# Kernel tuning notes

Hardware: AMD Instinct MI355X
Metric: run time of the kernel (lower is better)

The kernel has to match this reference:

```python
import jax, jax.numpy as jnp
import numpy as np

IN_FEATURE = 512
HID = 1024
N_EXPERTS = 16


def setup_inputs() -> dict:
    key = jax.random.key(0)
    ks = jax.random.split(key, 13)
    s_in = 1.0 / np.sqrt(IN_FEATURE)
    s_hid = 1.0 / np.sqrt(HID)
    x = jax.random.normal(ks[0], (8192, IN_FEATURE), dtype=jnp.float32)
    # Stacked expert params: expert i is Linear(in,hid)->silu->Linear(hid,hid)->silu->Linear(hid,1)
    W1 = jax.random.uniform(ks[1], (N_EXPERTS, IN_FEATURE, HID), jnp.float32, -s_in, s_in)
    b1 = jax.random.uniform(ks[2], (N_EXPERTS, HID), jnp.float32, -s_in, s_in)
    W2 = jax.random.uniform(ks[3], (N_EXPERTS, HID, HID), jnp.float32, -s_hid, s_hid)
    b2 = jax.random.uniform(ks[4], (N_EXPERTS, HID), jnp.float32, -s_hid, s_hid)
    W3 = jax.random.uniform(ks[5], (N_EXPERTS, HID), jnp.float32, -s_hid, s_hid)  # Linear(hid,1) weight, squeezed
    b3 = jax.random.uniform(ks[6], (N_EXPERTS,), jnp.float32, -s_hid, s_hid)
    # Gating params
    Wg1 = jax.random.uniform(ks[7], (IN_FEATURE, HID), jnp.float32, -s_in, s_in)
    bg1 = jax.random.uniform(ks[8], (HID,), jnp.float32, -s_in, s_in)
    Wg2 = jax.random.uniform(ks[9], (HID, HID), jnp.float32, -s_hid, s_hid)
    bg2 = jax.random.uniform(ks[10], (HID,), jnp.float32, -s_hid, s_hid)
    Wg3 = jax.random.uniform(ks[11], (HID, N_EXPERTS), jnp.float32, -s_hid, s_hid)
    bg3 = jax.random.uniform(ks[12], (N_EXPERTS,), jnp.float32, -s_hid, s_hid)
    return {"x": x, "W1": W1, "b1": b1, "W2": W2, "b2": b2, "W3": W3, "b3": b3,
            "Wg1": Wg1, "bg1": bg1, "Wg2": Wg2, "bg2": bg2, "Wg3": Wg3, "bg3": bg3}


def reference(x, W1, b1, W2, b2, W3, b3, Wg1, bg1, Wg2, bg2, Wg3, bg3):
    act = jax.nn.silu
    # Experts, batched over the expert axis: h [B, E, H]
    h = act(jnp.einsum('bi,eih->beh', x, W1) + b1)
    h = act(jnp.einsum('beh,ehk->bek', h, W2) + b2)
    expert_out = jnp.einsum('bek,ek->be', h, W3) + b3  # [B, E]
    # Gating network -> softmax over experts
    g = act(x @ Wg1 + bg1)
    g = act(g @ Wg2 + bg2)
    gate = jax.nn.softmax(g @ Wg3 + bg3, axis=1)  # [B, E]
    final = jnp.sum(expert_out * gate, axis=1).reshape(-1, 1)  # [B, 1]
    return final
```

## Files before the change

### kernel.cpp

```cpp
#include <hip/hip_runtime.h>

#define TOKENS 8192
#define INF 512
#define HIDDEN 1024
#define NEXP 16

typedef short bh4 __attribute__((ext_vector_type(4)));
typedef short bh8 __attribute__((ext_vector_type(8)));
typedef float f32x4 __attribute__((ext_vector_type(4)));

__device__ __forceinline__ short f2b(float f) {
  union { float f; unsigned u; } v; v.f = f;
  unsigned r = v.u + 0x7FFFu + ((v.u >> 16) & 1u);
  return (short)(r >> 16);
}
__device__ __forceinline__ float b2f(short h) {
  union { unsigned u; float f; } v; v.u = ((unsigned)(unsigned short)h) << 16;
  return v.f;
}
__device__ __forceinline__ float silu_f(float x) { return x / (1.f + __expf(-x)); }

__device__ __forceinline__ f32x4 mfma_16x16x32_bf16(bh8 a, bh8 b, f32x4 c) {
  asm("v_mfma_f32_16x16x32_bf16 %0, %1, %2, %0" : "+v"(c) : "v"(a), "v"(b));
  return c;
}

__global__ __launch_bounds__(256) void prep_kernel(
    const float* __restrict__ x, short* __restrict__ xb,
    const float* __restrict__ W1, short* __restrict__ W1t,
    const float* __restrict__ W2, short* __restrict__ W2t,
    const float* __restrict__ Wg1, short* __restrict__ Wg1t,
    const float* __restrict__ Wg2, short* __restrict__ Wg2t,
    float* __restrict__ eout) {
  __shared__ float tile[32][33];
  const int b = blockIdx.x;
  const int tid = threadIdx.x;

  if (b < 1024) {
    int nv = (TOKENS * INF) >> 2;
    int stride = 1024 * 256;
    for (int i = b * 256 + tid; i < nv; i += stride) {
      float4 v = ((const float4*)x)[i];
      bh4 o;
      o[0] = f2b(v.x); o[1] = f2b(v.y); o[2] = f2b(v.z); o[3] = f2b(v.w);
      *(bh4*)(xb + (size_t)i * 4) = o;
    }
    return;
  }
  if (b >= 27136) {
    int i = (b - 27136) * 256 + tid;
    f32x4 z; z[0] = 0.f; z[1] = 0.f; z[2] = 0.f; z[3] = 0.f;
    *(f32x4*)&eout[(size_t)i * 4] = z;
    return;
  }

  const float* src; short* dst; int R, C, bx, by; bool piDst;
  if (b < 9216) {
    int s = b - 1024; int zz = s >> 9; int rem = s & 511;
    bx = rem & 31; by = rem >> 5; R = INF; C = HIDDEN; piDst = false;
    src = W1 + (size_t)zz * R * C; dst = W1t + (size_t)zz * R * C;
  } else if (b < 25600) {
    int s = b - 9216; int zz = s >> 10; int rem = s & 1023;
    bx = rem & 31; by = rem >> 5; R = HIDDEN; C = HIDDEN; piDst = true;
    src = W2 + (size_t)zz * R * C; dst = W2t + (size_t)zz * R * C;
  } else if (b < 26112) {
    int s = b - 25600; bx = s & 31; by = s >> 5; R = INF; C = HIDDEN; piDst = false;
    src = Wg1; dst = Wg1t;
  } else {
    int s = b - 26112; bx = s & 31; by = s >> 5; R = HIDDEN; C = HIDDEN; piDst = true;
    src = Wg2; dst = Wg2t;
  }
  const int c0 = bx * 32, r0 = by * 32;
  {
    const int row = tid >> 3, col4 = (tid & 7) * 4;
    float4 v = *(const float4*)&src[(size_t)(r0 + row) * C + (c0 + col4)];
    tile[row][col4 + 0] = v.x; tile[row][col4 + 1] = v.y;
    tile[row][col4 + 2] = v.z; tile[row][col4 + 3] = v.w;
  }
  __syncthreads();
  {
    const int dc = tid >> 3, g = tid & 7;
    bh4 o;
    o[0] = f2b(tile[4 * g + 0][dc]); o[1] = f2b(tile[4 * g + 1][dc]);
    o[2] = f2b(tile[4 * g + 2][dc]); o[3] = f2b(tile[4 * g + 3][dc]);
    const int base = piDst ? ((g & 3) * 8 + (g >> 2) * 4) : (4 * g);
    *(bh4*)&dst[(size_t)(c0 + dc) * R + r0 + base] = o;
  }
}

__global__ __launch_bounds__(256, 4) void gemm_moe(
    const short* __restrict__ Abase, size_t aStride,
    const short* __restrict__ BtE, const short* __restrict__ BtG, size_t bStride,
    const float* __restrict__ biasE, const float* __restrict__ biasG,
    short* __restrict__ Cbase, size_t cStride,
    const float* __restrict__ W3all, float* __restrict__ eout,
    int jobBase, int K, int phase) {
  __shared__ short As[128][64];
  __shared__ short Bs[128][64];
  const int z = blockIdx.z;
  const int job = jobBase + z;
  const short* A = Abase + (size_t)z * aStride;
  const short* Bt = (job < NEXP) ? BtE + (size_t)job * bStride : BtG;
  const float* bias = (job < NEXP) ? biasE + (size_t)job * HIDDEN : biasG;

  const int bx = blockIdx.x, by = blockIdx.y;
  const int n0 = (by >> 3) * 128;
  const int m0 = (bx * 8 + (by & 7)) * 128;

  const int tid = threadIdx.x;
  const int lane = tid & 63;
  const int wid = tid >> 6;
  const int wm = (wid >> 1) * 64;
  const int wn = (wid & 1) * 64;
  const int quad = lane >> 4;
  const int l15 = lane & 15;

  f32x4 acc[4][4];
  #pragma unroll
  for (int i = 0; i < 4; ++i)
    #pragma unroll
    for (int j = 0; j < 4; ++j) {
      acc[i][j][0] = 0.f; acc[i][j][1] = 0.f; acc[i][j][2] = 0.f; acc[i][j][3] = 0.f;
    }

  const int srow = lane >> 3;
  const int scol = ((lane & 7) << 3) ^ (srow << 3);
  const short* aBase = A + (size_t)(m0 + wid * 32 + srow) * K + scol;
  const short* bBase = Bt + (size_t)(n0 + wid * 32 + srow) * K + scol;
  char* ldsA = (char*)&As[0][0];
  char* ldsB = (char*)&Bs[0][0];

  for (int kt = 0; kt < K; kt += 64) {
    __syncthreads();
    #pragma unroll
    for (int i = 0; i < 4; ++i) {
      __builtin_amdgcn_global_load_lds(
          (const __attribute__((address_space(1))) void*)(aBase + (size_t)(i * 8) * K + kt),
          (__attribute__((address_space(3))) void*)(ldsA + (wid * 4 + i) * 1024), 16, 0, 0);
      __builtin_amdgcn_global_load_lds(
          (const __attribute__((address_space(1))) void*)(bBase + (size_t)(i * 8) * K + kt),
          (__attribute__((address_space(3))) void*)(ldsB + (wid * 4 + i) * 1024), 16, 0, 0);
    }
    __syncthreads();

    #pragma unroll
    for (int ks = 0; ks < 2; ++ks) {
      bh8 af[4], bfr[4];
      #pragma unroll
      for (int mi = 0; mi < 4; ++mi) {
        int row = wm + mi * 16 + l15;
        int col = ((ks << 5) + (quad << 3)) ^ ((row & 7) << 3);
        af[mi] = *(const bh8*)&As[row][col];
      }
      #pragma unroll
      for (int ni = 0; ni < 4; ++ni) {
        int row = wn + ni * 16 + l15;
        int col = ((ks << 5) + (quad << 3)) ^ ((row & 7) << 3);
        bfr[ni] = *(const bh8*)&Bs[row][col];
      }
      #pragma unroll
      for (int mi = 0; mi < 4; ++mi)
        #pragma unroll
        for (int ni = 0; ni < 4; ++ni)
          acc[mi][ni] = mfma_16x16x32_bf16(bfr[ni], af[mi], acc[mi][ni]);
    }
  }

  if (phase == 1) {
    short* C = Cbase + (size_t)z * cStride;
    f32x4 bv4[4];
    #pragma unroll
    for (int ni = 0; ni < 4; ++ni)
      bv4[ni] = *(const f32x4*)&bias[n0 + wn + ni * 16 + quad * 4];
    #pragma unroll
    for (int mi = 0; mi < 4; ++mi) {
      int mrow = m0 + wm + mi * 16 + l15;
      #pragma unroll
      for (int blk = 0; blk < 2; ++blk) {
        bh8 o;
        #pragma unroll
        for (int r = 0; r < 4; ++r) {
          o[r]     = f2b(silu_f(acc[mi][blk * 2 + 0][r] + bv4[blk * 2 + 0][r]));
          o[r + 4] = f2b(silu_f(acc[mi][blk * 2 + 1][r] + bv4[blk * 2 + 1][r]));
        }
        *(bh8*)&C[(size_t)mrow * HIDDEN + n0 + wn + blk * 32 + quad * 8] = o;
      }
    }
  } else if (job == NEXP) {
    short* C = Cbase;
    #pragma unroll
    for (int ni = 0; ni < 4; ++ni) {
      int nb = wn + ni * 16 + quad * 4;
      float4 bv4 = *(const float4*)&bias[n0 + nb];
      #pragma unroll
      for (int mi = 0; mi < 4; ++mi) {
        int mrow = m0 + wm + mi * 16 + l15;
        bh4 o;
        o[0] = f2b(silu_f(acc[mi][ni][0] + bv4.x));
        o[1] = f2b(silu_f(acc[mi][ni][1] + bv4.y));
        o[2] = f2b(silu_f(acc[mi][ni][2] + bv4.z));
        o[3] = f2b(silu_f(acc[mi][ni][3] + bv4.w));
        *(bh4*)&C[(size_t)mrow * HIDDEN + n0 + nb] = o;
      }
    }
  } else {
    const float* w3 = W3all + (size_t)job * HIDDEN;
    float4 bv4[4], wv4[4];
    #pragma unroll
    for (int ni = 0; ni < 4; ++ni) {
      int nb = n0 + wn + ni * 16 + quad * 4;
      bv4[ni] = *(const float4*)&bias[nb];
      wv4[ni] = *(const float4*)&w3[nb];
    }
    #pragma unroll
    for (int mi = 0; mi < 4; ++mi) {
      float s = 0.f;
      #pragma unroll
      for (int ni = 0; ni < 4; ++ni) {
        s += silu_f(acc[mi][ni][0] + bv4[ni].x) * wv4[ni].x;
        s += silu_f(acc[mi][ni][1] + bv4[ni].y) * wv4[ni].y;
        s += silu_f(acc[mi][ni][2] + bv4[ni].z) * wv4[ni].z;
        s += silu_f(acc[mi][ni][3] + bv4[ni].w) * wv4[ni].w;
      }
      s += __shfl_xor(s, 16);
      s += __shfl_xor(s, 32);
      if (quad == 0) {
        int mrow = m0 + wm + mi * 16 + l15;
        atomicAdd(&eout[(size_t)mrow * NEXP + job], s);
      }
    }
  }
}

__global__ __launch_bounds__(256) void final_kernel(
    const short* __restrict__ g2b, const float* __restrict__ Wg3,
    const float* __restrict__ bg3, const float* __restrict__ eout,
    const float* __restrict__ b3, float* __restrict__ out) {
  int wave = (blockIdx.x * 256 + threadIdx.x) >> 6;
  int lane = threadIdx.x & 63;
  int r0 = wave * 4;
  float lp[4][16];
  #pragma unroll
  for (int r = 0; r < 4; ++r)
    #pragma unroll
    for (int j = 0; j < 16; ++j) lp[r][j] = 0.f;

  for (int t = 0; t < HIDDEN / 64; ++t) {
    int k = t * 64 + lane;
    float g0 = b2f(g2b[(size_t)(r0 + 0) * HIDDEN + k]);
    float g1 = b2f(g2b[(size_t)(r0 + 1) * HIDDEN + k]);
    float g2 = b2f(g2b[(size_t)(r0 + 2) * HIDDEN + k]);
    float g3 = b2f(g2b[(size_t)(r0 + 3) * HIDDEN + k]);
    const float4* wr4 = (const float4*)(Wg3 + (size_t)k * NEXP);
    float4 wa = wr4[0], wb = wr4[1], wc = wr4[2], wd = wr4[3];
    float w[16] = {wa.x, wa.y, wa.z, wa.w, wb.x, wb.y, wb.z, wb.w,
                   wc.x, wc.y, wc.z, wc.w, wd.x, wd.y, wd.z, wd.w};
    #pragma unroll
    for (int j = 0; j < 16; ++j) {
      lp[0][j] = fmaf(g0, w[j], lp[0][j]);
      lp[1][j] = fmaf(g1, w[j], lp[1][j]);
      lp[2][j] = fmaf(g2, w[j], lp[2][j]);
      lp[3][j] = fmaf(g3, w[j], lp[3][j]);
    }
  }
  #pragma unroll
  for (int r = 0; r < 4; ++r) {
    int row = r0 + r;
    float lpr[16];
    #pragma unroll
    for (int j = 0; j < 16; ++j) {
      float v = lp[r][j];
      v += __shfl_xor(v, 1);  v += __shfl_xor(v, 2);  v += __shfl_xor(v, 4);
      v += __shfl_xor(v, 8);  v += __shfl_xor(v, 16); v += __shfl_xor(v, 32);
      lpr[j] = v + bg3[j];
    }
    float mx = lpr[0];
    #pragma unroll
    for (int j = 1; j < 16; ++j) mx = fmaxf(mx, lpr[j]);
    float s = 0.f, accv = 0.f;
    #pragma unroll
    for (int j = 0; j < 16; ++j) {
      float p = __expf(lpr[j] - mx);
      s += p;
      accv = fmaf(p, eout[(size_t)row * NEXP + j] + b3[j], accv);
    }
    if (lane == 0) out[row] = accv / s;
  }
}

extern "C" void kernel_launch(void* const* d_in, const int* in_sizes, int n_in,
                              void* d_out, int out_size, void* d_ws, size_t ws_size,
                              hipStream_t stream) {
  const float* x   = (const float*)d_in[0];
  const float* W1  = (const float*)d_in[1];
  const float* b1  = (const float*)d_in[2];
  const float* W2  = (const float*)d_in[3];
  const float* b2  = (const float*)d_in[4];
  const float* W3  = (const float*)d_in[5];
  const float* b3  = (const float*)d_in[6];
  const float* Wg1 = (const float*)d_in[7];
  const float* bg1 = (const float*)d_in[8];
  const float* Wg2 = (const float*)d_in[9];
  const float* bg2 = (const float*)d_in[10];
  const float* Wg3 = (const float*)d_in[11];
  const float* bg3 = (const float*)d_in[12];
  float* out = (float*)d_out;

  char* p = (char*)d_ws;
  short* xb   = (short*)p; p += (size_t)TOKENS * INF * 2;
  short* W1t  = (short*)p; p += (size_t)NEXP * HIDDEN * INF * 2;
  short* W2t  = (short*)p; p += (size_t)NEXP * HIDDEN * HIDDEN * 2;
  short* Wg1t = (short*)p; p += (size_t)HIDDEN * INF * 2;
  short* Wg2t = (short*)p; p += (size_t)HIDDEN * HIDDEN * 2;
  short* g2b  = (short*)p; p += (size_t)TOKENS * HIDDEN * 2;
  float* eout = (float*)p; p += (size_t)TOKENS * NEXP * 4;
  size_t fixedBytes = (size_t)(p - (char*)d_ws);
  short* h1slab = (short*)p;
  const size_t SLOT_ELEMS = (size_t)TOKENS * HIDDEN;
  const size_t SLOT_BYTES = SLOT_ELEMS * 2;
  size_t avail = ws_size > fixedBytes ? ws_size - fixedBytes : 0;
  int slots = (int)(avail / SLOT_BYTES);
  if (slots > NEXP + 1) slots = NEXP + 1;
  if (slots < 1) slots = 1;

  prep_kernel<<<27264, 256, 0, stream>>>(x, xb, W1, W1t, W2, W2t, Wg1, Wg1t,
                                         Wg2, Wg2t, eout);

  for (int base = 0; base < NEXP + 1; base += slots) {
    int cnt = NEXP + 1 - base;
    if (cnt > slots) cnt = slots;
    dim3 gg(HIDDEN / 128, TOKENS / 128, cnt);
    gemm_moe<<<gg, 256, 0, stream>>>(xb, 0, W1t, Wg1t, (size_t)INF * HIDDEN,
                                     b1, bg1, h1slab, SLOT_ELEMS,
                                     nullptr, nullptr, base, INF, 1);
    gemm_moe<<<gg, 256, 0, stream>>>(h1slab, SLOT_ELEMS, W2t, Wg2t, (size_t)HIDDEN * HIDDEN,
                                     b2, bg2, g2b, 0,
                                     W3, eout, base, HIDDEN, 2);
  }

  final_kernel<<<TOKENS / 16, 256, 0, stream>>>(g2b, Wg3, bg3, eout, b3, out);
}
```

Measured before the change: 529.9 us.

## Double-buffer LDS tiles with K-step 32 to overlap loads and MFMA

The GEMM main loop now uses two LDS buffers of 128x32 per operand instead of one 128x64 buffer. Each iteration issues the next tile's global-to-LDS loads before running MFMAs on the current buffer, and the swizzle is changed to match the 32-wide rows. This aims to hide global load latency behind compute and needs one barrier per iteration instead of two. In exchange there are twice as many iterations, each doing half the MFMA work per barrier, while total LDS size stays the same.

```diff
diff --git a/kernel.cpp b/kernel.cpp
--- a/kernel.cpp
+++ b/kernel.cpp
@@ -4,6 +4,9 @@
 #define INF 512
 #define HIDDEN 1024
 #define NEXP 16
+
+#define AS1 __attribute__((address_space(1)))
+#define AS3 __attribute__((address_space(3)))
 
 typedef short bh4 __attribute__((ext_vector_type(4)));
 typedef short bh8 __attribute__((ext_vector_type(8)));
@@ -95,8 +98,8 @@
     short* __restrict__ Cbase, size_t cStride,
     const float* __restrict__ W3all, float* __restrict__ eout,
     int jobBase, int K, int phase) {
-  __shared__ short As[128][64];
-  __shared__ short Bs[128][64];
+  __shared__ short As[2][128][32];
+  __shared__ short Bs[2][128][32];
   const int z = blockIdx.z;
   const int job = jobBase + z;
   const short* A = Abase + (size_t)z * aStride;
@@ -123,47 +126,57 @@
       acc[i][j][0] = 0.f; acc[i][j][1] = 0.f; acc[i][j][2] = 0.f; acc[i][j][3] = 0.f;
     }
 
-  const int srow = lane >> 3;
-  const int scol = ((lane & 7) << 3) ^ (srow << 3);
-  const short* aBase = A + (size_t)(m0 + wid * 32 + srow) * K + scol;
-  const short* bBase = Bt + (size_t)(n0 + wid * 32 + srow) * K + scol;
-  char* ldsA = (char*)&As[0][0];
-  char* ldsB = (char*)&Bs[0][0];
-
-  for (int kt = 0; kt < K; kt += 64) {
+  const int srow = lane >> 2;
+  const int sg = ((lane & 3) ^ (srow & 3)) << 3;
+  const short* aB = A + (size_t)(m0 + wid * 32 + srow) * K + sg;
+  const short* bB = Bt + (size_t)(n0 + wid * 32 + srow) * K + sg;
+  char* ldsA = (char*)&As[0][0][0];
+  char* ldsB = (char*)&Bs[0][0][0];
+  const int dOff = (wid * 2) * 1024 + lane * 16;
+
+  const int nkt = K >> 5;
+
+  #pragma unroll
+  for (int i = 0; i < 2; ++i) {
+    __builtin_amdgcn_global_load_lds(
+        (const AS1 void*)(aB + (size_t)(16 * i) * K),
+        (AS3 void*)(ldsA + dOff + i * 1024), 16, 0, 0);
+    __builtin_amdgcn_global_load_lds(
+        (const AS1 void*)(bB + (size_t)(16 * i) * K),
+        (AS3 void*)(ldsB + dOff + i * 1024), 16, 0, 0);
+  }
+  __syncthreads();
+
+  const int pg = (quad ^ (l15 & 3)) << 3;
+  int buf = 0;
+  for (int t = 0; t < nkt; ++t) {
+    if (t + 1 < nkt) {
+      const int ktn = (t + 1) << 5;
+      const int dB = (buf ^ 1) * 8192 + dOff;
+      #pragma unroll
+      for (int i = 0; i < 2; ++i) {
+        __builtin_amdgcn_global_load_lds(
+            (const AS1 void*)(aB + (size_t)(16 * i) * K + ktn),
+            (AS3 void*)(ldsA + dB + i * 1024), 16, 0, 0);
+        __builtin_amdgcn_global_load_lds(
+            (const AS1 void*)(bB + (size_t)(16 * i) * K + ktn),
+            (AS3 void*)(ldsB + dB + i * 1024), 16, 0, 0);
+      }
+    }
+    bh8 af[4], bfr[4];
+    #pragma unroll
+    for (int mi = 0; mi < 4; ++mi)
+      af[mi] = *(const bh8*)&As[buf][wm + mi * 16 + l15][pg];
+    #pragma unroll
+    for (int ni = 0; ni < 4; ++ni)
+      bfr[ni] = *(const bh8*)&Bs[buf][wn + ni * 16 + l15][pg];
+    #pragma unroll
+    for (int mi = 0; mi < 4; ++mi)
+      #pragma unroll
+      for (int ni = 0; ni < 4; ++ni)
+        acc[mi][ni] = mfma_16x16x32_bf16(bfr[ni], af[mi], acc[mi][ni]);
     __syncthreads();
-    #pragma unroll
-    for (int i = 0; i < 4; ++i) {
-      __builtin_amdgcn_global_load_lds(
-          (const __attribute__((address_space(1))) void*)(aBase + (size_t)(i * 8) * K + kt),
-          (__attribute__((address_space(3))) void*)(ldsA + (wid * 4 + i) * 1024), 16, 0, 0);
-      __builtin_amdgcn_global_load_lds(
-          (const __attribute__((address_space(1))) void*)(bBase + (size_t)(i * 8) * K + kt),
-          (__attribute__((address_space(3))) void*)(ldsB + (wid * 4 + i) * 1024), 16, 0, 0);
-    }
-    __syncthreads();
-
-    #pragma unroll
-    for (int ks = 0; ks < 2; ++ks) {
-      bh8 af[4], bfr[4];
-      #pragma unroll
-      for (int mi = 0; mi < 4; ++mi) {
-        int row = wm + mi * 16 + l15;
-        int col = ((ks << 5) + (quad << 3)) ^ ((row & 7) << 3);
-        af[mi] = *(const bh8*)&As[row][col];
-      }
-      #pragma unroll
-      for (int ni = 0; ni < 4; ++ni) {
-        int row = wn + ni * 16 + l15;
-        int col = ((ks << 5) + (quad << 3)) ^ ((row & 7) << 3);
-        bfr[ni] = *(const bh8*)&Bs[row][col];
-      }
-      #pragma unroll
-      for (int mi = 0; mi < 4; ++mi)
-        #pragma unroll
-        for (int ni = 0; ni < 4; ++ni)
-          acc[mi][ni] = mfma_16x16x32_bf16(bfr[ni], af[mi], acc[mi][ni]);
-    }
+    buf ^= 1;
   }
 
   if (phase == 1) {
```

Result: slower. 630.1 us (+18.9%).
